# Optimization experiments

Measured on AMD Instinct MI355X. Metric: run time of the kernel, lower is better.

The kernel has to match this reference:

```python
import jax, jax.numpy as jnp
import numpy as np


def setup_inputs() -> dict:
    key = jax.random.key(0)
    k1, k2, k3, k4 = jax.random.split(key, 4)
    B, S, IN, OUT, ORG = 8, 4096, 1536, 3072, 4
    fan_in_std = (1.0 / IN) ** 0.5
    x = jax.random.normal(k1, (B, S, IN), dtype=jnp.float32)
    weight = jax.random.normal(k2, (ORG, IN, OUT), dtype=jnp.float32) * fan_in_std
    bias = jax.random.normal(k3, (ORG, OUT), dtype=jnp.float32) * 0.01
    organism_index = jax.random.randint(k4, (B,), 0, ORG, dtype=jnp.int64)
    return {"x": x, "organism_index": organism_index, "weight": weight, "bias": bias}


def reference(x, organism_index, weight, bias):
    # Gather per-sample weight [B, IN, OUT] and bias [B, OUT]
    w = weight[organism_index].astype(x.dtype)          # [B, IN, OUT]
    b = bias[organism_index].astype(x.dtype)            # [B, OUT]
    # x: [B, S, IN] -> [B, S, OUT]; bias broadcast over inner dims
    out = jnp.einsum('bsi,bij->bsj', x, w) + b[:, None, :]
    return out
```

## Files before the change

### kernel.cpp

```cpp
#include <hip/hip_runtime.h>
#include <hip/hip_bf16.h>
#include <stdint.h>

typedef __attribute__((ext_vector_type(4))) float f32x4;
typedef __attribute__((ext_vector_type(8))) short short8;

#define DIM_S 4096
#define DIM_IN 1536
#define DIM_OUT 3072
#define NB 8
#define NORG 4

#define XB_ELEMS (NB * DIM_S * DIM_IN)
#define WT_ELEMS (NORG * DIM_OUT * DIM_IN)
#define WS_NEED ((size_t)(XB_ELEMS + WT_ELEMS) * 2)

__device__ __forceinline__ unsigned short f2bf(float f) {
    union { __hip_bfloat16 h; unsigned short u; } c;
    c.h = __float2bfloat16(f);
    return c.u;
}

__device__ __forceinline__ void gload16(const void* g, void* l) {
    __builtin_amdgcn_global_load_lds(
        (const __attribute__((address_space(1))) unsigned int*)g,
        (__attribute__((address_space(3))) unsigned int*)l, 16, 0, 0);
}

__global__ __launch_bounds__(256) void cvt_x(const float* __restrict__ x,
                                             unsigned short* __restrict__ xb) {
    const int nchunk = XB_ELEMS / 8;
    for (int c = blockIdx.x * 256 + threadIdx.x; c < nchunk; c += gridDim.x * 256) {
        const float4 v0 = *reinterpret_cast<const float4*>(x + (size_t)c * 8);
        const float4 v1 = *reinterpret_cast<const float4*>(x + (size_t)c * 8 + 4);
        union { unsigned short u[8]; short8 v; } p;
        p.u[0] = f2bf(v0.x); p.u[1] = f2bf(v0.y); p.u[2] = f2bf(v0.z); p.u[3] = f2bf(v0.w);
        p.u[4] = f2bf(v1.x); p.u[5] = f2bf(v1.y); p.u[6] = f2bf(v1.z); p.u[7] = f2bf(v1.w);
        *reinterpret_cast<short8*>(xb + (size_t)c * 8) = p.v;
    }
}

__global__ __launch_bounds__(256) void cvt_wt(const float* __restrict__ w,
                                              unsigned short* __restrict__ wt) {
    __shared__ unsigned short T[64][68];
    const int bid = blockIdx.x;
    const int org = bid / (24 * 48);
    const int rem = bid % (24 * 48);
    const int k0 = (rem / 48) * 64;
    const int n0 = (rem % 48) * 64;
    const float* __restrict__ wp = w + (size_t)org * DIM_IN * DIM_OUT;
    unsigned short* __restrict__ op = wt + (size_t)org * DIM_OUT * DIM_IN;
    const int t = threadIdx.x;
    #pragma unroll
    for (int i = 0; i < 4; ++i) {
        const int c = t + 256 * i;
        const int kk = c >> 4, nq = (c & 15) * 4;
        const float4 v = *reinterpret_cast<const float4*>(
            wp + (size_t)(k0 + kk) * DIM_OUT + n0 + nq);
        ushort4 pv;
        pv.x = f2bf(v.x); pv.y = f2bf(v.y); pv.z = f2bf(v.z); pv.w = f2bf(v.w);
        *reinterpret_cast<ushort4*>(&T[kk][nq]) = pv;
    }
    __syncthreads();
    #pragma unroll
    for (int i = 0; i < 2; ++i) {
        const int c = t + 256 * i;
        const int n = c >> 3, k8 = (c & 7) * 8;
        union { unsigned short u[8]; short8 v; } p;
        #pragma unroll
        for (int j = 0; j < 8; ++j) p.u[j] = T[k8 + j][n];
        *reinterpret_cast<short8*>(op + (size_t)(n0 + n) * DIM_IN + k0 + k8) = p.v;
    }
}

__global__ __launch_bounds__(512, 2) void mol_gemm_8p(
    const unsigned short* __restrict__ xb, const int* __restrict__ orgidx,
    const unsigned short* __restrict__ wt, const float* __restrict__ bias,
    float* __restrict__ out)
{
    __shared__ __align__(16) unsigned short LDS[2][4][8192];

    const int tid  = threadIdx.x;
    const int lane = tid & 63;
    const int wave = tid >> 6;
    const int wr = wave >> 2;
    const int wc = wave & 3;
    const int l15 = lane & 15;
    const int q16 = lane >> 4;

    const int bid = blockIdx.x;
    const int id  = (bid & 7) * 192 + (bid >> 3);
    const int row0 = (id / 12) * 256;
    const int col0 = (id % 12) * 256;
    const int batch = row0 >> 12;
    const int org   = orgidx[batch];

    const unsigned short* __restrict__ Abase = xb + (size_t)row0 * DIM_IN;
    const unsigned short* __restrict__ Bbase =
        wt + (size_t)org * DIM_OUT * DIM_IN + (size_t)col0 * DIM_IN;

    const int rA = tid >> 2;
    const int qs = ((tid & 3) ^ (((tid >> 5) & 1) << 1)) * 8;
    const unsigned short* pA0 = Abase + (size_t)rA * DIM_IN + qs;
    const unsigned short* pA1 = Abase + (size_t)(128 + rA) * DIM_IN + qs;
    const unsigned short* pB0 = Bbase + (size_t)rA * DIM_IN + qs;
    const unsigned short* pB1 = Bbase + (size_t)(128 + rA) * DIM_IN + qs;

    const int d0 = wave * 512;
    const int d1 = 4096 + wave * 512;

    const int swb = ((l15 >> 3) & 1) << 1;
    const int offA0 = ((wr * 128 + l15) * 32 + ((q16 ^ swb) << 3)) * 2;
    const int offB0 = ((wc * 64  + l15) * 32 + ((q16 ^ swb) << 3)) * 2;
    const unsigned ldsbase = (unsigned)(unsigned long long)
        (const __attribute__((address_space(3))) unsigned short*)&LDS[0][0][0];
    const unsigned adrA = ldsbase + (unsigned)offA0;
    const unsigned adrB = ldsbase + (unsigned)offB0;

    f32x4 acc[8][4] = {};
    short8 af[2][4], bfr[2][4];

#define STG(buf, slot, p0, p1, kofs) do {                      \
        gload16((p0) + (kofs), &LDS[buf][slot][d0]);           \
        gload16((p1) + (kofs), &LDS[buf][slot][d1]);           \
    } while (0)

#define DSR(dst, addr, imm)                                                 \
    asm volatile("ds_read_b128 %0, %1 offset:%c2"                           \
                 : "=v"(dst) : "v"(addr), "i"(imm))

#define RD_A4(dst, buf, kk, mih) do {                                       \
        const unsigned aA_ = adrA +                                         \
            ((buf) * 65536u + (kk) * 16384u + (mih) * 4096u);               \
        DSR(af[dst][0], aA_, 0);    DSR(af[dst][1], aA_, 1024);             \
        DSR(af[dst][2], aA_, 2048); DSR(af[dst][3], aA_, 3072);             \
    } while (0)

#define RD_B4(dst, buf, kk) do {                                            \
        const unsigned aB_ = adrB +                                         \
            ((buf) * 65536u + (2 + (kk)) * 16384u);                         \
        DSR(bfr[dst][0], aB_, 0);    DSR(bfr[dst][1], aB_, 1024);           \
        DSR(bfr[dst][2], aB_, 2048); DSR(bfr[dst][3], aB_, 3072);           \
    } while (0)

#define MM(ca, cb, mih) do {                                                \
        __builtin_amdgcn_s_setprio(1);                                      \
        _Pragma("unroll")                                                   \
        for (int i_ = 0; i_ < 4; ++i_) {                                    \
            _Pragma("unroll")                                               \
            for (int n_ = 0; n_ < 4; ++n_)                                  \
                acc[(mih)*4 + i_][n_] =                                     \
                    __builtin_amdgcn_mfma_f32_16x16x32_bf16(                \
                        af[ca][i_], bfr[cb][n_],                            \
                        acc[(mih)*4 + i_][n_], 0, 0, 0);                    \
        }                                                                   \
        __builtin_amdgcn_s_setprio(0);                                      \
    } while (0)

#define BAR  do { __builtin_amdgcn_s_barrier();                             \
                  asm volatile("" ::: "memory"); } while (0)
#define WAIT4 asm volatile("s_waitcnt vmcnt(4)" ::: "memory")
#define WAIT8 asm volatile("s_waitcnt vmcnt(8)" ::: "memory")
#define WAITL(n) do { asm volatile("s_waitcnt lgkmcnt(" #n ")");            \
                      __builtin_amdgcn_sched_barrier(0); } while (0)
#define KADV(k) do { if ((k) < 1504) (k) += 32; } while (0)

    STG(0, 0, pA0, pA1, 0);
    STG(0, 2, pB0, pB1, 0);
    STG(0, 1, pA0, pA1, 32);
    STG(0, 3, pB0, pB1, 32);
    STG(1, 0, pA0, pA1, 64);
    STG(1, 2, pB0, pB1, 64);
    WAIT8;
    BAR;
    RD_A4(0, 0, 0, 0);
    RD_B4(0, 0, 0);

    int kA = 96, kB = 96;

#define TILE2() do {                                                          \
   STG(1,1,pA0,pA1,kA); KADV(kA); RD_A4(1, 0,0,1);                      \
         WAITL(4); MM(0,0,0);                 BAR;                            \
   STG(1,3,pB0,pB1,kB); KADV(kB); RD_A4(0, 0,1,0); RD_B4(1, 0,1);      \
         WAITL(8); MM(1,0,1);          WAIT4; BAR;                            \
   STG(0,0,pA0,pA1,kA); KADV(kA); RD_A4(1, 0,1,1);                      \
         WAITL(4); MM(0,1,0);                 BAR;                            \
   STG(0,2,pB0,pB1,kB); KADV(kB); RD_A4(0, 1,0,0); RD_B4(0, 1,0);      \
         WAITL(8); MM(1,1,1);          WAIT4; BAR;                            \
   STG(0,1,pA0,pA1,kA); KADV(kA); RD_A4(1, 1,0,1);                      \
         WAITL(4); MM(0,0,0);                 BAR;                            \
   STG(0,3,pB0,pB1,kB); KADV(kB); RD_A4(0, 1,1,0); RD_B4(1, 1,1);      \
         WAITL(8); MM(1,0,1);          WAIT4; BAR;                            \
   STG(1,0,pA0,pA1,kA); KADV(kA); RD_A4(1, 1,1,1);                      \
         WAITL(4); MM(0,1,0);                 BAR;                            \
   STG(1,2,pB0,pB1,kB); KADV(kB); RD_A4(0, 0,0,0); RD_B4(0, 0,0);      \
         WAITL(8); MM(1,1,1);          WAIT4; BAR;                            \
} while (0)

    #pragma unroll 1
    for (int i = 0; i < 12; ++i) {
        TILE2();
    }

    asm volatile("s_waitcnt lgkmcnt(0)");

    const float* __restrict__ bptr = bias + (size_t)org * DIM_OUT;
    const int crow = q16 * 4;
    const int ccol = l15;
    #pragma unroll
    for (int ni = 0; ni < 4; ++ni) {
        const int gc = col0 + wc * 64 + ni * 16 + ccol;
        const float bv = bptr[gc];
        #pragma unroll
        for (int mi = 0; mi < 8; ++mi) {
            const int gr = row0 + wr * 128 + mi * 16 + crow;
            #pragma unroll
            for (int r = 0; r < 4; ++r)
                out[(size_t)(gr + r) * DIM_OUT + gc] = acc[mi][ni][r] + bv;
        }
    }
#undef STG
#undef DSR
#undef RD_A4
#undef RD_B4
#undef MM
#undef BAR
#undef WAIT4
#undef WAIT8
#undef WAITL
#undef KADV
#undef TILE2
}

#define BM 128
#define BN 128
#define BK 32
#define LDK 40
union BF8 { unsigned short u[8]; short8 v; };

__global__ __launch_bounds__(256) void mol_gemm_fb(
    const float* __restrict__ x, const int* __restrict__ orgidx,
    const float* __restrict__ weight, const float* __restrict__ bias,
    float* __restrict__ out)
{
    __shared__ __align__(16) unsigned short Alds[2][BM][LDK];
    __shared__ __align__(16) unsigned short Blds[2][BN][LDK];

    const int tid  = threadIdx.x;
    const int lane = tid & 63;
    const int wave = tid >> 6;
    const int wr = wave >> 1, wc = wave & 1;

    const int bid = blockIdx.x;
    const int id  = (bid & 7) * 768 + (bid >> 3);
    const int row0 = (id / 24) * BM;
    const int col0 = (id % 24) * BN;

    const int batch = row0 / DIM_S;
    const int org   = orgidx[batch];
    const float* __restrict__ W = weight + (size_t)org * DIM_IN * DIM_OUT;

    f32x4 acc[4][4] = {};
    const int ar  = tid >> 2;
    const int ak8 = (tid & 3) * 8;
    const int bn  = tid & 127;
    const int bg0 = tid >> 7;
    const float* __restrict__ xbase = x + (size_t)row0 * DIM_IN;
    const float* __restrict__ wbase = W + col0 + bn;

    auto stage = [&](int buf, int k0) {
        #pragma unroll
        for (int i = 0; i < 2; ++i) {
            const int r = ar + 64 * i;
            const float* xp = xbase + (size_t)r * DIM_IN + k0 + ak8;
            const float4 v0 = *reinterpret_cast<const float4*>(xp);
            const float4 v1 = *reinterpret_cast<const float4*>(xp + 4);
            BF8 p;
            p.u[0] = f2bf(v0.x); p.u[1] = f2bf(v0.y);
            p.u[2] = f2bf(v0.z); p.u[3] = f2bf(v0.w);
            p.u[4] = f2bf(v1.x); p.u[5] = f2bf(v1.y);
            p.u[6] = f2bf(v1.z); p.u[7] = f2bf(v1.w);
            *reinterpret_cast<short8*>(&Alds[buf][r][ak8]) = p.v;
        }
        #pragma unroll
        for (int j = 0; j < 2; ++j) {
            const int g = bg0 + 2 * j;
            const float* wp = wbase + (size_t)(k0 + 8 * g) * DIM_OUT;
            BF8 p;
            #pragma unroll
            for (int r = 0; r < 8; ++r) p.u[r] = f2bf(wp[(size_t)r * DIM_OUT]);
            *reinterpret_cast<short8*>(&Blds[buf][bn][8 * g]) = p.v;
        }
    };

    stage(0, 0);
    const int nk = DIM_IN / BK;
    const int kq = (lane >> 4) * 8;
    const int lr = lane & 15;

    for (int t = 0; t < nk; ++t) {
        __syncthreads();
        const int cur = t & 1;
        if (t + 1 < nk) stage(cur ^ 1, (t + 1) * BK);
        short8 a[4], b[4];
        #pragma unroll
        for (int mi = 0; mi < 4; ++mi)
            a[mi] = *reinterpret_cast<const short8*>(&Alds[cur][wr * 64 + mi * 16 + lr][kq]);
        #pragma unroll
        for (int ni = 0; ni < 4; ++ni)
            b[ni] = *reinterpret_cast<const short8*>(&Blds[cur][wc * 64 + ni * 16 + lr][kq]);
        #pragma unroll
        for (int mi = 0; mi < 4; ++mi)
            #pragma unroll
            for (int ni = 0; ni < 4; ++ni)
                acc[mi][ni] = __builtin_amdgcn_mfma_f32_16x16x32_bf16(
                    a[mi], b[ni], acc[mi][ni], 0, 0, 0);
    }

    const float* __restrict__ bptr = bias + (size_t)org * DIM_OUT;
    const int crow = (lane >> 4) * 4;
    const int ccol = lane & 15;
    #pragma unroll
    for (int ni = 0; ni < 4; ++ni) {
        const int gc = col0 + wc * 64 + ni * 16 + ccol;
        const float bv = bptr[gc];
        #pragma unroll
        for (int mi = 0; mi < 4; ++mi) {
            const int gr = row0 + wr * 64 + mi * 16 + crow;
            #pragma unroll
            for (int r = 0; r < 4; ++r)
                out[(size_t)(gr + r) * DIM_OUT + gc] = acc[mi][ni][r] + bv;
        }
    }
}

extern "C" void kernel_launch(void* const* d_in, const int* in_sizes, int n_in,
                              void* d_out, int out_size, void* d_ws, size_t ws_size,
                              hipStream_t stream)
{
    const float* x      = (const float*)d_in[0];
    const int*   orgidx = (const int*)d_in[1];
    const float* weight = (const float*)d_in[2];
    const float* bias   = (const float*)d_in[3];
    float* out = (float*)d_out;

    if (ws_size >= WS_NEED) {
        unsigned short* xbp = (unsigned short*)d_ws;
        unsigned short* wtp = xbp + XB_ELEMS;
        cvt_x<<<dim3(2048), dim3(256), 0, stream>>>(x, xbp);
        cvt_wt<<<dim3(NORG * 24 * 48), dim3(256), 0, stream>>>(weight, wtp);
        mol_gemm_8p<<<dim3(1536), dim3(512), 0, stream>>>(xbp, orgidx, wtp, bias, out);
    } else {
        mol_gemm_fb<<<dim3(6144), dim3(256), 0, stream>>>(x, orgidx, weight, bias, out);
    }
}
```

Baseline: 430.1 us.

## Remap tiles per XCD by batch and merge A/B stage loads

```diff
diff --git a/kernel.cpp b/kernel.cpp
--- a/kernel.cpp
+++ b/kernel.cpp
@@ -89,11 +89,14 @@
     const int q16 = lane >> 4;
 
     const int bid = blockIdx.x;
-    const int id  = (bid & 7) * 192 + (bid >> 3);
-    const int row0 = (id / 12) * 256;
-    const int col0 = (id % 12) * 256;
-    const int batch = row0 >> 12;
-    const int org   = orgidx[batch];
+    const int xcd = bid & 7;
+    const int lid = bid >> 3;
+    const int sc  = lid >> 5;
+    const int r16 = (lid >> 1) & 15;
+    const int c2  = lid & 1;
+    const int row0 = (xcd * 16 + r16) * 256;
+    const int col0 = (sc * 2 + c2) * 256;
+    const int org  = orgidx[xcd];
 
     const unsigned short* __restrict__ Abase = xb + (size_t)row0 * DIM_IN;
     const unsigned short* __restrict__ Bbase =
@@ -120,9 +123,11 @@
     f32x4 acc[8][4] = {};
     short8 af[2][4], bfr[2][4];
 
-#define STG(buf, slot, p0, p1, kofs) do {                      \
-        gload16((p0) + (kofs), &LDS[buf][slot][d0]);           \
-        gload16((p1) + (kofs), &LDS[buf][slot][d1]);           \
+#define STG2(buf, kk, kofs) do {                               \
+        gload16(pA0 + (kofs), &LDS[buf][kk][d0]);              \
+        gload16(pA1 + (kofs), &LDS[buf][kk][d1]);              \
+        gload16(pB0 + (kofs), &LDS[buf][2 + (kk)][d0]);        \
+        gload16(pB1 + (kofs), &LDS[buf][2 + (kk)][d1]);        \
     } while (0)
 
 #define DSR(dst, addr, imm)                                                 \
@@ -159,42 +164,38 @@
 
 #define BAR  do { __builtin_amdgcn_s_barrier();                             \
                   asm volatile("" ::: "memory"); } while (0)
-#define WAIT4 asm volatile("s_waitcnt vmcnt(4)" ::: "memory")
 #define WAIT8 asm volatile("s_waitcnt vmcnt(8)" ::: "memory")
 #define WAITL(n) do { asm volatile("s_waitcnt lgkmcnt(" #n ")");            \
                       __builtin_amdgcn_sched_barrier(0); } while (0)
 #define KADV(k) do { if ((k) < 1504) (k) += 32; } while (0)
 
-    STG(0, 0, pA0, pA1, 0);
-    STG(0, 2, pB0, pB1, 0);
-    STG(0, 1, pA0, pA1, 32);
-    STG(0, 3, pB0, pB1, 32);
-    STG(1, 0, pA0, pA1, 64);
-    STG(1, 2, pB0, pB1, 64);
+    STG2(0, 0, 0);
+    STG2(0, 1, 32);
+    STG2(1, 0, 64);
     WAIT8;
     BAR;
     RD_A4(0, 0, 0, 0);
     RD_B4(0, 0, 0);
 
-    int kA = 96, kB = 96;
+    int kS = 96;
 
 #define TILE2() do {                                                          \
-   STG(1,1,pA0,pA1,kA); KADV(kA); RD_A4(1, 0,0,1);                      \
-         WAITL(4); MM(0,0,0);                 BAR;                            \
-   STG(1,3,pB0,pB1,kB); KADV(kB); RD_A4(0, 0,1,0); RD_B4(1, 0,1);      \
-         WAITL(8); MM(1,0,1);          WAIT4; BAR;                            \
-   STG(0,0,pA0,pA1,kA); KADV(kA); RD_A4(1, 0,1,1);                      \
-         WAITL(4); MM(0,1,0);                 BAR;                            \
-   STG(0,2,pB0,pB1,kB); KADV(kB); RD_A4(0, 1,0,0); RD_B4(0, 1,0);      \
-         WAITL(8); MM(1,1,1);          WAIT4; BAR;                            \
-   STG(0,1,pA0,pA1,kA); KADV(kA); RD_A4(1, 1,0,1);                      \
-         WAITL(4); MM(0,0,0);                 BAR;                            \
-   STG(0,3,pB0,pB1,kB); KADV(kB); RD_A4(0, 1,1,0); RD_B4(1, 1,1);      \
-         WAITL(8); MM(1,0,1);          WAIT4; BAR;                            \
-   STG(1,0,pA0,pA1,kA); KADV(kA); RD_A4(1, 1,1,1);                      \
-         WAITL(4); MM(0,1,0);                 BAR;                            \
-   STG(1,2,pB0,pB1,kB); KADV(kB); RD_A4(0, 0,0,0); RD_B4(0, 0,0);      \
-         WAITL(8); MM(1,1,1);          WAIT4; BAR;                            \
+   STG2(1,1,kS); KADV(kS); RD_A4(1, 0,0,1);                             \
+         WAITL(4); MM(0,0,0); WAIT8; BAR;                                     \
+   RD_A4(0, 0,1,0); RD_B4(1, 0,1);                                      \
+         WAITL(8); MM(1,0,1); BAR;                                            \
+   STG2(0,0,kS); KADV(kS); RD_A4(1, 0,1,1);                             \
+         WAITL(4); MM(0,1,0); WAIT8; BAR;                                     \
+   RD_A4(0, 1,0,0); RD_B4(0, 1,0);                                      \
+         WAITL(8); MM(1,1,1); BAR;                                            \
+   STG2(0,1,kS); KADV(kS); RD_A4(1, 1,0,1);                             \
+         WAITL(4); MM(0,0,0); WAIT8; BAR;                                     \
+   RD_A4(0, 1,1,0); RD_B4(1, 1,1);                                      \
+         WAITL(8); MM(1,0,1); BAR;                                            \
+   STG2(1,0,kS); KADV(kS); RD_A4(1, 1,1,1);                             \
+         WAITL(4); MM(0,1,0); WAIT8; BAR;                                     \
+   RD_A4(0, 0,0,0); RD_B4(0, 0,0);                                      \
+         WAITL(8); MM(1,1,1); BAR;                                            \
 } while (0)
 
     #pragma unroll 1
@@ -219,13 +220,12 @@
                 out[(size_t)(gr + r) * DIM_OUT + gc] = acc[mi][ni][r] + bv;
         }
     }
-#undef STG
+#undef STG2
 #undef DSR
 #undef RD_A4
 #undef RD_B4
 #undef MM
 #undef BAR
-#undef WAIT4
 #undef WAIT8
 #undef WAITL
 #undef KADV
```

Result: slower. 459.5 us (+6.8%).

## Switch GEMM to 32x32x16 MFMA and merge conversion kernels into one launch

Applied to the files above, without the earlier changes.

```diff
diff --git a/kernel.cpp b/kernel.cpp
--- a/kernel.cpp
+++ b/kernel.cpp
@@ -2,8 +2,9 @@
 #include <hip/hip_bf16.h>
 #include <stdint.h>
 
-typedef __attribute__((ext_vector_type(4))) float f32x4;
-typedef __attribute__((ext_vector_type(8))) short short8;
+typedef __attribute__((ext_vector_type(4)))  float f32x4;
+typedef __attribute__((ext_vector_type(16))) float f32x16;
+typedef __attribute__((ext_vector_type(8)))  short short8;
 
 #define DIM_S 4096
 #define DIM_IN 1536
@@ -14,6 +15,8 @@
 #define XB_ELEMS (NB * DIM_S * DIM_IN)
 #define WT_ELEMS (NORG * DIM_OUT * DIM_IN)
 #define WS_NEED ((size_t)(XB_ELEMS + WT_ELEMS) * 2)
+#define NWT_BLOCKS (NORG * 24 * 48)
+#define NX_BLOCKS 2048
 
 __device__ __forceinline__ unsigned short f2bf(float f) {
     union { __hip_bfloat16 h; unsigned short u; } c;
@@ -27,49 +30,51 @@
         (__attribute__((address_space(3))) unsigned int*)l, 16, 0, 0);
 }
 
-__global__ __launch_bounds__(256) void cvt_x(const float* __restrict__ x,
-                                             unsigned short* __restrict__ xb) {
-    const int nchunk = XB_ELEMS / 8;
-    for (int c = blockIdx.x * 256 + threadIdx.x; c < nchunk; c += gridDim.x * 256) {
-        const float4 v0 = *reinterpret_cast<const float4*>(x + (size_t)c * 8);
-        const float4 v1 = *reinterpret_cast<const float4*>(x + (size_t)c * 8 + 4);
-        union { unsigned short u[8]; short8 v; } p;
-        p.u[0] = f2bf(v0.x); p.u[1] = f2bf(v0.y); p.u[2] = f2bf(v0.z); p.u[3] = f2bf(v0.w);
-        p.u[4] = f2bf(v1.x); p.u[5] = f2bf(v1.y); p.u[6] = f2bf(v1.z); p.u[7] = f2bf(v1.w);
-        *reinterpret_cast<short8*>(xb + (size_t)c * 8) = p.v;
-    }
-}
-
-__global__ __launch_bounds__(256) void cvt_wt(const float* __restrict__ w,
-                                              unsigned short* __restrict__ wt) {
-    __shared__ unsigned short T[64][68];
-    const int bid = blockIdx.x;
-    const int org = bid / (24 * 48);
-    const int rem = bid % (24 * 48);
-    const int k0 = (rem / 48) * 64;
-    const int n0 = (rem % 48) * 64;
-    const float* __restrict__ wp = w + (size_t)org * DIM_IN * DIM_OUT;
-    unsigned short* __restrict__ op = wt + (size_t)org * DIM_OUT * DIM_IN;
+__global__ __launch_bounds__(256) void cvt_all(const float* __restrict__ x,
+                                               const float* __restrict__ w,
+                                               unsigned short* __restrict__ xb,
+                                               unsigned short* __restrict__ wt) {
     const int t = threadIdx.x;
-    #pragma unroll
-    for (int i = 0; i < 4; ++i) {
-        const int c = t + 256 * i;
-        const int kk = c >> 4, nq = (c & 15) * 4;
-        const float4 v = *reinterpret_cast<const float4*>(
-            wp + (size_t)(k0 + kk) * DIM_OUT + n0 + nq);
-        ushort4 pv;
-        pv.x = f2bf(v.x); pv.y = f2bf(v.y); pv.z = f2bf(v.z); pv.w = f2bf(v.w);
-        *reinterpret_cast<ushort4*>(&T[kk][nq]) = pv;
-    }
-    __syncthreads();
-    #pragma unroll
-    for (int i = 0; i < 2; ++i) {
-        const int c = t + 256 * i;
-        const int n = c >> 3, k8 = (c & 7) * 8;
-        union { unsigned short u[8]; short8 v; } p;
-        #pragma unroll
-        for (int j = 0; j < 8; ++j) p.u[j] = T[k8 + j][n];
-        *reinterpret_cast<short8*>(op + (size_t)(n0 + n) * DIM_IN + k0 + k8) = p.v;
+    if (blockIdx.x < NWT_BLOCKS) {
+        __shared__ unsigned short T[64][68];
+        const int bid = blockIdx.x;
+        const int org = bid / (24 * 48);
+        const int rem = bid % (24 * 48);
+        const int k0 = (rem / 48) * 64;
+        const int n0 = (rem % 48) * 64;
+        const float* __restrict__ wp = w + (size_t)org * DIM_IN * DIM_OUT;
+        unsigned short* __restrict__ op = wt + (size_t)org * DIM_OUT * DIM_IN;
+        #pragma unroll
+        for (int i = 0; i < 4; ++i) {
+            const int c = t + 256 * i;
+            const int kk = c >> 4, nq = (c & 15) * 4;
+            const float4 v = *reinterpret_cast<const float4*>(
+                wp + (size_t)(k0 + kk) * DIM_OUT + n0 + nq);
+            ushort4 pv;
+            pv.x = f2bf(v.x); pv.y = f2bf(v.y); pv.z = f2bf(v.z); pv.w = f2bf(v.w);
+            *reinterpret_cast<ushort4*>(&T[kk][nq]) = pv;
+        }
+        __syncthreads();
+        #pragma unroll
+        for (int i = 0; i < 2; ++i) {
+            const int c = t + 256 * i;
+            const int n = c >> 3, k8 = (c & 7) * 8;
+            union { unsigned short u[8]; short8 v; } p;
+            #pragma unroll
+            for (int j = 0; j < 8; ++j) p.u[j] = T[k8 + j][n];
+            *reinterpret_cast<short8*>(op + (size_t)(n0 + n) * DIM_IN + k0 + k8) = p.v;
+        }
+    } else {
+        const int nchunk = XB_ELEMS / 8;
+        const int xb0 = blockIdx.x - NWT_BLOCKS;
+        for (int c = xb0 * 256 + t; c < nchunk; c += NX_BLOCKS * 256) {
+            const float4 v0 = *reinterpret_cast<const float4*>(x + (size_t)c * 8);
+            const float4 v1 = *reinterpret_cast<const float4*>(x + (size_t)c * 8 + 4);
+            union { unsigned short u[8]; short8 v; } p;
+            p.u[0] = f2bf(v0.x); p.u[1] = f2bf(v0.y); p.u[2] = f2bf(v0.z); p.u[3] = f2bf(v0.w);
+            p.u[4] = f2bf(v1.x); p.u[5] = f2bf(v1.y); p.u[6] = f2bf(v1.z); p.u[7] = f2bf(v1.w);
+            *reinterpret_cast<short8*>(xb + (size_t)c * 8) = p.v;
+        }
     }
 }
 
@@ -85,15 +90,14 @@
     const int wave = tid >> 6;
     const int wr = wave >> 2;
     const int wc = wave & 3;
-    const int l15 = lane & 15;
-    const int q16 = lane >> 4;
+    const int l31 = lane & 31;
+    const int lhi = lane >> 5;
 
     const int bid = blockIdx.x;
     const int id  = (bid & 7) * 192 + (bid >> 3);
     const int row0 = (id / 12) * 256;
     const int col0 = (id % 12) * 256;
-    const int batch = row0 >> 12;
-    const int org   = orgidx[batch];
+    const int org  = orgidx[row0 >> 12];
 
     const unsigned short* __restrict__ Abase = xb + (size_t)row0 * DIM_IN;
     const unsigned short* __restrict__ Bbase =
@@ -109,15 +113,17 @@
     const int d0 = wave * 512;
     const int d1 = 4096 + wave * 512;
 
-    const int swb = ((l15 >> 3) & 1) << 1;
-    const int offA0 = ((wr * 128 + l15) * 32 + ((q16 ^ swb) << 3)) * 2;
-    const int offB0 = ((wc * 64  + l15) * 32 + ((q16 ^ swb) << 3)) * 2;
+    const int sflip = (l31 >> 3) & 1;
     const unsigned ldsbase = (unsigned)(unsigned long long)
         (const __attribute__((address_space(3))) unsigned short*)&LDS[0][0][0];
-    const unsigned adrA = ldsbase + (unsigned)offA0;
-    const unsigned adrB = ldsbase + (unsigned)offB0;
-
-    f32x4 acc[8][4] = {};
+    const unsigned rbA = ldsbase + (unsigned)((wr * 128 + l31) * 64 + lhi * 16);
+    const unsigned rbB = ldsbase + (unsigned)((wc * 64  + l31) * 64 + lhi * 16);
+    const unsigned adrA_ks0 = rbA + (unsigned)(sflip * 32);
+    const unsigned adrA_ks1 = rbA + (unsigned)(32 - sflip * 32);
+    const unsigned adrB_ks0 = rbB + (unsigned)(sflip * 32);
+    const unsigned adrB_ks1 = rbB + (unsigned)(32 - sflip * 32);
+
+    f32x16 acc[4][2] = {};
     short8 af[2][4], bfr[2][4];
 
 #define STG(buf, slot, p0, p1, kofs) do {                      \
@@ -130,29 +136,50 @@
                  : "=v"(dst) : "v"(addr), "i"(imm))
 
 #define RD_A4(dst, buf, kk, mih) do {                                       \
-        const unsigned aA_ = adrA +                                         \
-            ((buf) * 65536u + (kk) * 16384u + (mih) * 4096u);               \
-        DSR(af[dst][0], aA_, 0);    DSR(af[dst][1], aA_, 1024);             \
-        DSR(af[dst][2], aA_, 2048); DSR(af[dst][3], aA_, 3072);             \
+        const unsigned o_ = (buf) * 65536u + (kk) * 16384u;                 \
+        DSR(af[dst][0], adrA_ks0, ((mih)*2 + 0) * 2048);                    \
+        asm volatile("ds_read_b128 %0, %1 offset:%c2"                       \
+            : "=v"(af[dst][1]) : "v"(adrA_ks1 + o_), "i"(((mih)*2+0)*2048));\
+        asm volatile("ds_read_b128 %0, %1 offset:%c2"                       \
+            : "=v"(af[dst][2]) : "v"(adrA_ks0 + o_), "i"(((mih)*2+1)*2048));\
+        asm volatile("ds_read_b128 %0, %1 offset:%c2"                       \
+            : "=v"(af[dst][3]) : "v"(adrA_ks1 + o_), "i"(((mih)*2+1)*2048));\
+    } while (0)
+
+#undef RD_A4
+#define RD_A4(dst, buf, kk, mih) do {                                       \
+        const unsigned o0_ = adrA_ks0 + (buf) * 65536u + (kk) * 16384u;     \
+        const unsigned o1_ = adrA_ks1 + (buf) * 65536u + (kk) * 16384u;     \
+        DSR(af[dst][0], o0_, ((mih)*2 + 0) * 2048);                         \
+        DSR(af[dst][1], o1_, ((mih)*2 + 0) * 2048);                         \
+        DSR(af[dst][2], o0_, ((mih)*2 + 1) * 2048);                         \
+        DSR(af[dst][3], o1_, ((mih)*2 + 1) * 2048);                         \
     } while (0)
 
 #define RD_B4(dst, buf, kk) do {                                            \
-        const unsigned aB_ = adrB +                                         \
-            ((buf) * 65536u + (2 + (kk)) * 16384u);                         \
-        DSR(bfr[dst][0], aB_, 0);    DSR(bfr[dst][1], aB_, 1024);           \
-        DSR(bfr[dst][2], aB_, 2048); DSR(bfr[dst][3], aB_, 3072);           \
+        const unsigned o0_ = adrB_ks0 + (buf) * 65536u + (2+(kk)) * 16384u; \
+        const unsigned o1_ = adrB_ks1 + (buf) * 65536u + (2+(kk)) * 16384u; \
+        DSR(bfr[dst][0], o0_, 0);                                           \
+        DSR(bfr[dst][1], o1_, 0);                                           \
+        DSR(bfr[dst][2], o0_, 2048);                                        \
+        DSR(bfr[dst][3], o1_, 2048);                                        \
     } while (0)
 
 #define MM(ca, cb, mih) do {                                                \
         __builtin_amdgcn_s_setprio(1);                                      \
         _Pragma("unroll")                                                   \
-        for (int i_ = 0; i_ < 4; ++i_) {                                    \
+        for (int ml_ = 0; ml_ < 2; ++ml_) {                                 \
             _Pragma("unroll")                                               \
-            for (int n_ = 0; n_ < 4; ++n_)                                  \
-                acc[(mih)*4 + i_][n_] =                                     \
-                    __builtin_amdgcn_mfma_f32_16x16x32_bf16(                \
-                        af[ca][i_], bfr[cb][n_],                            \
-                        acc[(mih)*4 + i_][n_], 0, 0, 0);                    \
+            for (int nf_ = 0; nf_ < 2; ++nf_) {                             \
+                acc[(mih)*2 + ml_][nf_] =                                   \
+                    __builtin_amdgcn_mfma_f32_32x32x16_bf16(                \
+                        af[ca][ml_*2 + 0], bfr[cb][nf_*2 + 0],              \
+                        acc[(mih)*2 + ml_][nf_], 0, 0, 0);                  \
+                acc[(mih)*2 + ml_][nf_] =                                   \
+                    __builtin_amdgcn_mfma_f32_32x32x16_bf16(                \
+                        af[ca][ml_*2 + 1], bfr[cb][nf_*2 + 1],              \
+                        acc[(mih)*2 + ml_][nf_], 0, 0, 0);                  \
+            }                                                               \
         }                                                                   \
         __builtin_amdgcn_s_setprio(0);                                      \
     } while (0)
@@ -205,18 +232,18 @@
     asm volatile("s_waitcnt lgkmcnt(0)");
 
     const float* __restrict__ bptr = bias + (size_t)org * DIM_OUT;
-    const int crow = q16 * 4;
-    const int ccol = l15;
     #pragma unroll
-    for (int ni = 0; ni < 4; ++ni) {
-        const int gc = col0 + wc * 64 + ni * 16 + ccol;
+    for (int nf = 0; nf < 2; ++nf) {
+        const int gc = col0 + wc * 64 + nf * 32 + l31;
         const float bv = bptr[gc];
         #pragma unroll
-        for (int mi = 0; mi < 8; ++mi) {
-            const int gr = row0 + wr * 128 + mi * 16 + crow;
-            #pragma unroll
-            for (int r = 0; r < 4; ++r)
-                out[(size_t)(gr + r) * DIM_OUT + gc] = acc[mi][ni][r] + bv;
+        for (int mf = 0; mf < 4; ++mf) {
+            const int grb = row0 + wr * 128 + mf * 32 + 4 * lhi;
+            #pragma unroll
+            for (int reg = 0; reg < 16; ++reg) {
+                const int gr = grb + (reg & 3) + 8 * (reg >> 2);
+                out[(size_t)gr * DIM_OUT + gc] = acc[mf][nf][reg] + bv;
+            }
         }
     }
 #undef STG
@@ -347,8 +374,8 @@
     if (ws_size >= WS_NEED) {
         unsigned short* xbp = (unsigned short*)d_ws;
         unsigned short* wtp = xbp + XB_ELEMS;
-        cvt_x<<<dim3(2048), dim3(256), 0, stream>>>(x, xbp);
-        cvt_wt<<<dim3(NORG * 24 * 48), dim3(256), 0, stream>>>(weight, wtp);
+        cvt_all<<<dim3(NWT_BLOCKS + NX_BLOCKS), dim3(256), 0, stream>>>(
+            x, weight, xbp, wtp);
         mol_gemm_8p<<<dim3(1536), dim3(512), 0, stream>>>(xbp, orgidx, wtp, bias, out);
     } else {
         mol_gemm_fb<<<dim3(6144), dim3(256), 0, stream>>>(x, orgidx, weight, bias, out);
```

Result: faster. 402.0 us (-6.5%).
